# Performance work log

Hardware: AMD Instinct MI355X
Metric: run time of the kernel (lower is better)

The kernel has to match this reference:

```python
import jax, jax.numpy as jnp
import numpy as np

# (dy, dx) offsets corresponding to the single -1 entries of kernels 1..8
# delta1 rows: (0,0),(0,1),(0,2),(1,2); delta2 = spatial flip: (2,2),(2,1),(2,0),(1,0)
OFFSETS = [(-1, -1), (-1, 0), (-1, 1), (0, 1), (1, 1), (1, 0), (1, -1), (0, -1)]
NUM_LAYER = 9
EPS = 1e-12


def _shift(x, dy, dx):
    # zero-padded shift: out[y, x] = in[y + dy, x + dx]; dilation = shifts[0] = 1
    b, c, h, w = x.shape
    p = jnp.pad(x, ((0, 0), (0, 0), (1, 1), (1, 1)))
    return jax.lax.dynamic_slice(p, (0, 0, 1 + dy, 1 + dx), (b, c, h, w))


def _l2norm(v, axis):
    # matches torch.nn.functional.normalize: v / max(||v||, eps)
    n = jnp.sqrt(jnp.sum(v * v, axis=axis, keepdims=True))
    return v / jnp.maximum(n, EPS)


def setup_inputs() -> dict:
    key = jax.random.key(0)
    k1, k2, k3, k4 = jax.random.split(key, 4)
    B, C, H, W = 4, 256, 96, 96
    cen = jax.random.normal(k1, (B, C, H, W), dtype=jnp.float32)
    scale = 1.0 / np.sqrt(C)
    # grouped 1x1 convs (groups=9): per-group (C x C) weight matrices
    W1 = jax.random.normal(k2, (NUM_LAYER, C, C), dtype=jnp.float32) * scale
    W2 = jax.random.normal(k3, (C, C), dtype=jnp.float32) * scale
    W3 = jax.random.normal(k4, (NUM_LAYER, C, C), dtype=jnp.float32) * scale
    return {"cen": cen, "W1": W1, "W2": W2, "W3": W3}


def reference(cen, W1, W2, W3):
    b, c, h, w = cen.shape
    # Extract_layer: 8 fixed depthwise 3x3 convs (each = negated shift) + identity
    surrounds = jnp.stack(
        [-_shift(cen, dy, dx) for dy, dx in OFFSETS] + [cen], axis=1
    )  # (b, 9, c, h, w)
    # Analyze_layer: grouped 1x1 convs = per-group matmuls
    out1 = jnp.einsum("gij,bgjhw->bgihw", W1, surrounds)
    out2 = jnp.einsum("ij,bjhw->bihw", W2, cen)[:, None]  # (b, 1, c, h, w)
    out3 = jnp.einsum("gij,bgjhw->bgihw", W3, surrounds)
    out1 = _l2norm(out1, axis=2)
    out2 = _l2norm(out2, axis=2)
    out3 = _l2norm(out3, axis=2)
    # softmax over a size-1 axis (dim=2 after mean+keepdim) -> identically 1.0
    att = jax.nn.softmax(
        jnp.mean(out1 * out2, axis=2, keepdims=True), axis=2
    )  # (b, 9, 1, h, w)
    out = jnp.sum(att * out3, axis=1)  # (b, c, h, w)
    return out + cen
```

## Files before the change

kernel.cpp:

```cpp
#include <hip/hip_runtime.h>
#include <stdint.h>

#define BB 4
#define CC 256
#define HH 96
#define WW 96
#define HP 98
#define CP 264
#define XT 32
#define YT 6
#define XE 34

typedef __bf16 bf16x8 __attribute__((ext_vector_type(8)));
typedef __bf16 bf16x16 __attribute__((ext_vector_type(16)));
typedef float f32x4 __attribute__((ext_vector_type(4)));
typedef float f32x16 __attribute__((ext_vector_type(16)));

__device__ __forceinline__ uint16_t f2bf(float f) {
    uint32_t u = __float_as_uint(f);
    u += 0x7FFFu + ((u >> 16) & 1u);
    return (uint16_t)(u >> 16);
}

__global__ void zero_halo(uint16_t* __restrict__ cenT) {
    int idx = blockIdx.x * 256 + threadIdx.x;
    if (idx >= 1552 * 33) return;
    int p = idx / 33, q = idx - p * 33;
    int b = p / 388, s = p - b * 388;
    int y, x;
    if (s < 98)      { y = 0;       x = s; }
    else if (s < 196){ y = 97;      x = s - 98; }
    else if (s < 292){ x = 0;       y = s - 196 + 1; }
    else             { x = 97;      y = s - 292 + 1; }
    size_t o = (((size_t)b * HP + y) * HP + x) * CP + q * 8;
    *(uint4*)(cenT + o) = make_uint4(0u, 0u, 0u, 0u);
}

__global__ void transpose_cen(const float* __restrict__ cen, uint16_t* __restrict__ cenT) {
    const int y = blockIdx.x, b = blockIdx.y, ch = blockIdx.z, tid = threadIdx.x;
    __shared__ uint16_t ldsX[128 * 100];

    #pragma unroll
    for (int i = 0; i < 12; ++i) {
        int f = i * 256 + tid;
        int c = f / 24, xq = f % 24;
        float4 v = *(const float4*)(cen + ((((size_t)b * CC + ch * 128 + c) * HH + y) * WW + xq * 4));
        uint2 pk;
        pk.x = (uint32_t)f2bf(v.x) | ((uint32_t)f2bf(v.y) << 16);
        pk.y = (uint32_t)f2bf(v.z) | ((uint32_t)f2bf(v.w) << 16);
        *(uint2*)(&ldsX[c * 100 + xq * 4]) = pk;
    }
    __syncthreads();
    #pragma unroll
    for (int i = 0; i < 6; ++i) {
        int t = i * 256 + tid;
        int x = t % 96, cq = t / 96;
        uint32_t w0, w1, w2, w3;
        w0 = (uint32_t)ldsX[(cq * 8 + 0) * 100 + x] | ((uint32_t)ldsX[(cq * 8 + 1) * 100 + x] << 16);
        w1 = (uint32_t)ldsX[(cq * 8 + 2) * 100 + x] | ((uint32_t)ldsX[(cq * 8 + 3) * 100 + x] << 16);
        w2 = (uint32_t)ldsX[(cq * 8 + 4) * 100 + x] | ((uint32_t)ldsX[(cq * 8 + 5) * 100 + x] << 16);
        w3 = (uint32_t)ldsX[(cq * 8 + 6) * 100 + x] | ((uint32_t)ldsX[(cq * 8 + 7) * 100 + x] << 16);
        size_t o = (((size_t)b * HP + (y + 1)) * HP + (x + 1)) * CP + ch * 128 + cq * 8;
        *(uint4*)(cenT + o) = make_uint4(w0, w1, w2, w3);
    }
}

__global__ void cvt_w3(const float* __restrict__ W3, uint16_t* __restrict__ W3bf) {
    int e = (blockIdx.x * 256 + threadIdx.x) * 4;
    int g = e >> 16, n = (e >> 8) & 255, k = e & 255;
    float4 v = *(const float4*)(W3 + e);
    uint2 pk;
    pk.x = (uint32_t)f2bf(v.x) | ((uint32_t)f2bf(v.y) << 16);
    pk.y = (uint32_t)f2bf(v.z) | ((uint32_t)f2bf(v.w) << 16);
    size_t o = (size_t)(((g * 8 + (n >> 5)) * 16 + (k >> 4)) * 512)
             + (n & 31) * 16 + ((k >> 3) & 1) * 8 + (k & 7);
    *(uint2*)(W3bf + o) = pk;
}

__global__ __launch_bounds__(512, 2)
void ecm_main(const float* __restrict__ cen, const uint16_t* __restrict__ cenT,
              const uint16_t* __restrict__ W3bf, float* __restrict__ out) {
    const int tid = threadIdx.x;
    const int wv = tid >> 6, lane = tid & 63, col = lane & 31, kh = lane >> 5;
    const int c2 = wv & 3, p3 = wv >> 2;
    const int x0 = blockIdx.x * XT, y0 = blockIdx.y * YT, b = blockIdx.z;

    __shared__ __align__(16) uint16_t ldsA[8 * XE * CP];
    __shared__ __align__(16) float ldsP[2][192][4];

    const int dgOrd[9] = {0, 1, 2, 7, 8, 3, 6, 5, 4};

    for (int rr = 0; rr < 8; ++rr) {
        const uint4* gs = (const uint4*)(cenT + (((size_t)b * HP + (y0 + rr)) * HP + x0) * CP);
        uint4* ls = (uint4*)(ldsA + rr * XE * CP);
        for (int c = tid; c < XE * CP / 8; c += 512) ls[c] = gs[c];
    }
    __syncthreads();

    const uint16_t* wbA = W3bf + (size_t)(2 * c2) * (16 * 512) + col * 16 + kh * 8;
    bf16x16 fA[3] = {}, fB[3] = {};

    #pragma unroll 1
    for (int idx = 0; idx < 9; ++idx) {
        const int g = dgOrd[idx], dg = idx / 3, dx = idx % 3 - 1;

        const uint16_t* wgA = wbA + (size_t)g * 65536;
        const uint16_t* wgB = wgA + 16 * 512;
        int a[3];
        #pragma unroll
        for (int rr = 0; rr < 3; ++rr)
            a[rr] = ((dg + 3 * p3 + rr) * XE + (col + dx + 1)) * CP + kh * 8;

        f32x16 aA[3] = {}, aB[3] = {};

        bf16x8 qA[2], qB[2];
        qA[0] = *(const bf16x8*)(wgA);
        qB[0] = *(const bf16x8*)(wgB);
        qA[1] = *(const bf16x8*)(wgA + 512);
        qB[1] = *(const bf16x8*)(wgB + 512);
        bf16x8 bR[3];
        #pragma unroll
        for (int rr = 0; rr < 3; ++rr) bR[rr] = *(const bf16x8*)(ldsA + a[rr]);

        #pragma unroll
        for (int ks = 0; ks < 16; ++ks) {
            bf16x8 wa = qA[ks & 1], wb = qB[ks & 1];
            if (ks + 2 < 16) {
                qA[ks & 1] = *(const bf16x8*)(wgA + (ks + 2) * 512);
                qB[ks & 1] = *(const bf16x8*)(wgB + (ks + 2) * 512);
            }
            bf16x8 bN[3];
            #pragma unroll
            for (int rr = 0; rr < 3; ++rr)
                bN[rr] = (ks + 1 < 16) ? *(const bf16x8*)(ldsA + a[rr] + (ks + 1) * 16)
                                       : bR[rr];
            __builtin_amdgcn_s_setprio(1);
            #pragma unroll
            for (int rr = 0; rr < 3; ++rr) {
                aA[rr] = __builtin_amdgcn_mfma_f32_32x32x16_bf16(wa, bR[rr], aA[rr], 0, 0, 0);
                aB[rr] = __builtin_amdgcn_mfma_f32_32x32x16_bf16(wb, bR[rr], aB[rr], 0, 0, 0);
            }
            __builtin_amdgcn_s_setprio(0);
            #pragma unroll
            for (int rr = 0; rr < 3; ++rr) bR[rr] = bN[rr];
        }

        float s[3];
        #pragma unroll
        for (int rr = 0; rr < 3; ++rr) {
            float t = 0.f;
            #pragma unroll
            for (int r = 0; r < 16; ++r) t += aA[rr][r] * aA[rr][r] + aB[rr][r] * aB[rr][r];
            t += __shfl_xor(t, 32, 64);
            s[rr] = t;
        }
        if (kh == 0) {
            #pragma unroll
            for (int rr = 0; rr < 3; ++rr)
                ldsP[idx & 1][(3 * p3 + rr) * 32 + col][c2] = s[rr];
        }
        __syncthreads();

        const float sgn = (g == 8) ? 1.f : -1.f;
        #pragma unroll
        for (int rr = 0; rr < 3; ++rr) {
            f32x4 pa = *(const f32x4*)&ldsP[idx & 1][(3 * p3 + rr) * 32 + col][0];
            float n = pa[0] + pa[1] + pa[2] + pa[3];
            float sc = sgn / fmaxf(sqrtf(n), 1e-12f);
            #pragma unroll
            for (int r = 0; r < 16; ++r) {
                fA[rr][r] = (__bf16)((float)fA[rr][r] + aA[rr][r] * sc);
                fB[rr][r] = (__bf16)((float)fB[rr][r] + aB[rr][r] * sc);
            }
        }
    }

    #pragma unroll
    for (int rr = 0; rr < 3; ++rr) {
        #pragma unroll
        for (int r = 0; r < 16; ++r) {
            int chA = c2 * 64 + (r & 3) + 8 * (r >> 2) + 4 * kh;
            size_t oA = (((size_t)b * CC + chA) * HH + (y0 + 3 * p3 + rr)) * WW + (x0 + col);
            out[oA] = (float)fA[rr][r] + cen[oA];
            size_t oB = oA + (size_t)32 * HH * WW;
            out[oB] = (float)fB[rr][r] + cen[oB];
        }
    }
}

extern "C" void kernel_launch(void* const* d_in, const int* in_sizes, int n_in,
                              void* d_out, int out_size, void* d_ws, size_t ws_size,
                              hipStream_t stream) {
    const float* cen = (const float*)d_in[0];
    const float* W3 = (const float*)d_in[3];
    float* out = (float*)d_out;

    uint16_t* cenT = (uint16_t*)d_ws;
    const size_t cenT_elems = (size_t)BB * HP * HP * CP;
    uint16_t* W3bf = cenT + cenT_elems;

    zero_halo<<<201, 256, 0, stream>>>(cenT);
    transpose_cen<<<dim3(HH, BB, 2), 256, 0, stream>>>(cen, cenT);
    cvt_w3<<<576, 256, 0, stream>>>(W3, W3bf);
    ecm_main<<<dim3(3, 16, 4), 512, 0, stream>>>(cen, cenT, W3bf, out);
}
```

Baseline: 160.8 us.

## Remap waves to one 32-channel slice across all six rows

Each of the eight waves now owns a single 32-output-channel slice and computes all six rows of the tile, instead of a 64-channel pair over three rows. This halves the weight fragment loads per wave and doubles the reuse of each weight fragment, but each wave now reads six LDS activation fragments per k-step instead of three. The software prefetch of the LDS B fragments is dropped, and the norm partial sums are reduced over eight waves. The change trades global weight traffic for more LDS reads and exposed LDS latency.

```diff
diff --git a/kernel.cpp b/kernel.cpp
--- a/kernel.cpp
+++ b/kernel.cpp
@@ -82,11 +82,10 @@
               const uint16_t* __restrict__ W3bf, float* __restrict__ out) {
     const int tid = threadIdx.x;
     const int wv = tid >> 6, lane = tid & 63, col = lane & 31, kh = lane >> 5;
-    const int c2 = wv & 3, p3 = wv >> 2;
     const int x0 = blockIdx.x * XT, y0 = blockIdx.y * YT, b = blockIdx.z;
 
     __shared__ __align__(16) uint16_t ldsA[8 * XE * CP];
-    __shared__ __align__(16) float ldsP[2][192][4];
+    __shared__ __align__(16) float ldsP[2][192][8];
 
     const int dgOrd[9] = {0, 1, 2, 7, 8, 3, 6, 5, 4};
 
@@ -97,93 +96,70 @@
     }
     __syncthreads();
 
-    const uint16_t* wbA = W3bf + (size_t)(2 * c2) * (16 * 512) + col * 16 + kh * 8;
-    bf16x16 fA[3] = {}, fB[3] = {};
+    const uint16_t* wbA = W3bf + (size_t)wv * (16 * 512) + col * 16 + kh * 8;
+    bf16x16 fin[6] = {};
 
     #pragma unroll 1
     for (int idx = 0; idx < 9; ++idx) {
         const int g = dgOrd[idx], dg = idx / 3, dx = idx % 3 - 1;
 
         const uint16_t* wgA = wbA + (size_t)g * 65536;
-        const uint16_t* wgB = wgA + 16 * 512;
-        int a[3];
+        int a[6];
         #pragma unroll
-        for (int rr = 0; rr < 3; ++rr)
-            a[rr] = ((dg + 3 * p3 + rr) * XE + (col + dx + 1)) * CP + kh * 8;
+        for (int rr = 0; rr < 6; ++rr)
+            a[rr] = ((dg + rr) * XE + (col + dx + 1)) * CP + kh * 8;
 
-        f32x16 aA[3] = {}, aB[3] = {};
+        f32x16 acc[6] = {};
 
-        bf16x8 qA[2], qB[2];
+        bf16x8 qA[2];
         qA[0] = *(const bf16x8*)(wgA);
-        qB[0] = *(const bf16x8*)(wgB);
         qA[1] = *(const bf16x8*)(wgA + 512);
-        qB[1] = *(const bf16x8*)(wgB + 512);
-        bf16x8 bR[3];
-        #pragma unroll
-        for (int rr = 0; rr < 3; ++rr) bR[rr] = *(const bf16x8*)(ldsA + a[rr]);
 
         #pragma unroll
         for (int ks = 0; ks < 16; ++ks) {
-            bf16x8 wa = qA[ks & 1], wb = qB[ks & 1];
-            if (ks + 2 < 16) {
-                qA[ks & 1] = *(const bf16x8*)(wgA + (ks + 2) * 512);
-                qB[ks & 1] = *(const bf16x8*)(wgB + (ks + 2) * 512);
-            }
-            bf16x8 bN[3];
+            bf16x8 wa = qA[ks & 1];
+            if (ks + 2 < 16) qA[ks & 1] = *(const bf16x8*)(wgA + (ks + 2) * 512);
+            bf16x8 br[6];
             #pragma unroll
-            for (int rr = 0; rr < 3; ++rr)
-                bN[rr] = (ks + 1 < 16) ? *(const bf16x8*)(ldsA + a[rr] + (ks + 1) * 16)
-                                       : bR[rr];
+            for (int rr = 0; rr < 6; ++rr)
+                br[rr] = *(const bf16x8*)(ldsA + a[rr] + ks * 16);
             __builtin_amdgcn_s_setprio(1);
             #pragma unroll
-            for (int rr = 0; rr < 3; ++rr) {
-                aA[rr] = __builtin_amdgcn_mfma_f32_32x32x16_bf16(wa, bR[rr], aA[rr], 0, 0, 0);
-                aB[rr] = __builtin_amdgcn_mfma_f32_32x32x16_bf16(wb, bR[rr], aB[rr], 0, 0, 0);
-            }
+            for (int rr = 0; rr < 6; ++rr)
+                acc[rr] = __builtin_amdgcn_mfma_f32_32x32x16_bf16(wa, br[rr], acc[rr], 0, 0, 0);
             __builtin_amdgcn_s_setprio(0);
-            #pragma unroll
-            for (int rr = 0; rr < 3; ++rr) bR[rr] = bN[rr];
         }
 
-        float s[3];
         #pragma unroll
-        for (int rr = 0; rr < 3; ++rr) {
+        for (int rr = 0; rr < 6; ++rr) {
             float t = 0.f;
             #pragma unroll
-            for (int r = 0; r < 16; ++r) t += aA[rr][r] * aA[rr][r] + aB[rr][r] * aB[rr][r];
+            for (int r = 0; r < 16; ++r) t += acc[rr][r] * acc[rr][r];
             t += __shfl_xor(t, 32, 64);
-            s[rr] = t;
-        }
-        if (kh == 0) {
-            #pragma unroll
-            for (int rr = 0; rr < 3; ++rr)
-                ldsP[idx & 1][(3 * p3 + rr) * 32 + col][c2] = s[rr];
+            if (kh == 0) ldsP[idx & 1][rr * 32 + col][wv] = t;
         }
         __syncthreads();
 
         const float sgn = (g == 8) ? 1.f : -1.f;
         #pragma unroll
-        for (int rr = 0; rr < 3; ++rr) {
-            f32x4 pa = *(const f32x4*)&ldsP[idx & 1][(3 * p3 + rr) * 32 + col][0];
-            float n = pa[0] + pa[1] + pa[2] + pa[3];
+        for (int rr = 0; rr < 6; ++rr) {
+            f32x4 pa = *(const f32x4*)&ldsP[idx & 1][rr * 32 + col][0];
+            f32x4 pb = *(const f32x4*)&ldsP[idx & 1][rr * 32 + col][4];
+            float n = pa[0] + pa[1] + pa[2] + pa[3] + pb[0] + pb[1] + pb[2] + pb[3];
             float sc = sgn / fmaxf(sqrtf(n), 1e-12f);
             #pragma unroll
-            for (int r = 0; r < 16; ++r) {
-                fA[rr][r] = (__bf16)((float)fA[rr][r] + aA[rr][r] * sc);
-                fB[rr][r] = (__bf16)((float)fB[rr][r] + aB[rr][r] * sc);
-            }
+            for (int r = 0; r < 16; ++r)
+                fin[rr][r] = (__bf16)((float)fin[rr][r] + acc[rr][r] * sc);
         }
     }
 
     #pragma unroll
-    for (int rr = 0; rr < 3; ++rr) {
+    for (int rr = 0; rr < 6; ++rr) {
         #pragma unroll
         for (int r = 0; r < 16; ++r) {
-            int chA = c2 * 64 + (r & 3) + 8 * (r >> 2) + 4 * kh;
-            size_t oA = (((size_t)b * CC + chA) * HH + (y0 + 3 * p3 + rr)) * WW + (x0 + col);
-            out[oA] = (float)fA[rr][r] + cen[oA];
-            size_t oB = oA + (size_t)32 * HH * WW;
-            out[oB] = (float)fB[rr][r] + cen[oB];
+            int ch = wv * 32 + (r & 3) + 8 * (r >> 2) + 4 * kh;
+            size_t o = (((size_t)b * CC + ch) * HH + (y0 + rr)) * WW + (x0 + col);
+            out[o] = (float)fin[rr][r] + cen[o];
         }
     }
 }
```

New measurement: 163.2 us. About the same (+1.5%).
